# Performance work log

Measured on AMD Instinct MI355X. Metric: run time of the kernel, lower is better.

The kernel has to match this reference:

```python
import jax, jax.numpy as jnp
import numpy as np

L_MAX = 6
R = 1
IN_IRREPS  = [(256,0),(128,1),(128,2),(64,3),(64,4),(64,5),(64,6)]
HID_IRREPS = [(64,0),(64,1),(64,2),(32,3),(32,4),(32,5),(32,6)]
N_SCALARS = 64
N_GATES = sum(m for m, l in HID_IRREPS if l > 0)  # 256
PRE_IRREPS = [(N_SCALARS,0),(N_GATES,0)] + [(m,l) for m,l in HID_IRREPS if l > 0]
OUT_IRREPS = [(R,l) for l in range(L_MAX+1)]

def _dim(irr):
    return sum(m*(2*l+1) for m, l in irr)

def _wsize(in_irr, out_irr):
    mul_in = {l: m for m, l in in_irr}
    return sum(mul_in[l]*mo for mo, l in out_irr)

def e3linear(x, wflat, in_irr, out_irr):
    # block-diagonal per-irrep linear with e3nn 1/sqrt(fan_in) normalization
    B = x.shape[0]
    blocks = {}
    off = 0
    for mul, l in in_irr:
        d = mul*(2*l+1)
        blocks[l] = (x[:, off:off+d].reshape(B, mul, 2*l+1), mul)
        off += d
    outs = []
    woff = 0
    for mul_out, l in out_irr:
        xb, mul_in = blocks[l]
        w = wflat[woff:woff+mul_in*mul_out].reshape(mul_in, mul_out)
        woff += mul_in*mul_out
        y = jnp.einsum('bim,io->bom', xb, w) * (1.0/np.sqrt(mul_in))
        outs.append(y.reshape(B, mul_out*(2*l+1)))
    return jnp.concatenate(outs, axis=1)

def gate(z):
    # z = [scalars 64x0e | gates 256x0e | gated l>0 irreps]
    s = jax.nn.silu(z[:, :N_SCALARS])
    g = jax.nn.sigmoid(z[:, N_SCALARS:N_SCALARS+N_GATES])
    x = z[:, N_SCALARS+N_GATES:]
    outs = [s]
    goff = 0
    xoff = 0
    for mul, l in HID_IRREPS:
        if l == 0:
            continue
        m = 2*l+1
        xb = x[:, xoff:xoff+mul*m].reshape(-1, mul, m)
        outs.append((xb * g[:, goff:goff+mul, None]).reshape(-1, mul*m))
        goff += mul
        xoff += mul*m
    return jnp.concatenate(outs, axis=1)

def _forward(v_raw, w1, w2, w3, w4):
    x = gate(e3linear(v_raw, w1, IN_IRREPS, PRE_IRREPS))
    x = gate(e3linear(x, w2, HID_IRREPS, PRE_IRREPS))
    x = gate(e3linear(x, w3, HID_IRREPS, PRE_IRREPS))
    c = e3linear(x, w4, HID_IRREPS, OUT_IRREPS)  # [B, 49]
    B = c.shape[0]
    segs = []
    off = 0
    for l in range(L_MAX+1):
        m = 2*l+1
        seg = c[:, off:off+R*m].reshape(B, R, m).transpose(0, 2, 1)  # (B, m, R)
        segs.append(seg)
        off += R*m
    return jnp.concatenate(segs, axis=1)  # (B, 49, R)

def setup_inputs():
    key = jax.random.key(0)
    ks = jax.random.split(key, 5)
    B = 16384
    return {
        "v_raw": jax.random.normal(ks[0], (B, _dim(IN_IRREPS)), jnp.float32),
        "w1": jax.random.normal(ks[1], (_wsize(IN_IRREPS, PRE_IRREPS),), jnp.float32),
        "w2": jax.random.normal(ks[2], (_wsize(HID_IRREPS, PRE_IRREPS),), jnp.float32),
        "w3": jax.random.normal(ks[3], (_wsize(HID_IRREPS, PRE_IRREPS),), jnp.float32),
        "w4": jax.random.normal(ks[4], (_wsize(HID_IRREPS, OUT_IRREPS),), jnp.float32),
    }

def reference(v_raw, w1, w2, w3, w4):
    return _forward(v_raw, w1, w2, w3, w4)
```

## Files before the change

kernel.cpp:

```cpp
#include <hip/hip_runtime.h>
#include <cstddef>


typedef _Float16 half8 __attribute__((ext_vector_type(8)));
typedef _Float16 half4 __attribute__((ext_vector_type(4)));
typedef float    f32x4 __attribute__((ext_vector_type(4)));
typedef float    fvec4 __attribute__((ext_vector_type(4)));

#define B_ROWS   16
#define IN_DIM   3840
#define OUT_COLS 49
#define GP  264
#define HSP 72

#define OFF_G1  0
#define OFF_G2  4224
#define OFF_G3  8448
#define OFF_HS1 12672
#define OFF_HS2 13824
#define SMEM_ELTS 14976

#define P2BASE 106496
#define P3BASE 139264

__global__ __launch_bounds__(256) void prep_weights(
    const float* __restrict__ w1, const float* __restrict__ w2,
    const float* __restrict__ w3, _Float16* __restrict__ packed)
{
  static const int K_[24]    = {256,256,128,128,64,64,64,64,  64,64,64,64,32,32,32,32,
                                64,64,64,64,32,32,32,32};
  static const int N_[24]    = {64,256,64,64,32,32,32,32,  64,256,64,64,32,32,32,32,
                                64,256,64,64,32,32,32,32};
  static const int woff_[24] = {0,16384,81920,90112,98304,100352,102400,104448,
                                0,4096,20480,24576,28672,29696,30720,31744,
                                0,4096,20480,24576,28672,29696,30720,31744};
  static const int poff_[24] = {0,16384,81920,90112,98304,100352,102400,104448,
                                106496,110592,126976,131072,135168,136192,137216,138240,
                                139264,143360,159744,163840,167936,168960,169984,171008};
  const int g = blockIdx.x * 256 + threadIdx.x;
  int bi = 0;
#pragma unroll
  for (int i = 1; i < 24; ++i) if (g * 8 >= poff_[i]) bi = i;
  const float* w = (bi < 8) ? w1 : ((bi < 16) ? w2 : w3);
  const int rel8 = g - poff_[bi] / 8;
  const int K = K_[bi], N = N_[bi];
  const float scale = 1.0f / sqrtf((float)K);
  half8 vv;
  if (bi < 8) {
    const int lane = rel8 & 63;
    const int fi   = rel8 >> 6;
    const int KF = K >> 5;
    const int kf = fi % KF;
    const int mt = fi / KF;
    const int k0 = kf * 32 + (lane >> 4) * 8;
    const int o  = mt * 16 + (lane & 15);
#pragma unroll
    for (int j = 0; j < 8; ++j)
      vv[j] = (_Float16)(w[woff_[bi] + (size_t)(k0 + j) * N + o] * scale);
  } else {
    const int f  = rel8 >> 5;
    const int lp = (rel8 & 31) << 1;
    const int KF16 = K >> 4;
    const int ks = f % KF16;
    const int mt = f / KF16;
#pragma unroll
    for (int t = 0; t < 2; ++t) {
      const int l  = lp + t;
      const int i0 = ks * 16 + (l >> 4) * 4;
      const int o  = mt * 16 + (l & 15);
#pragma unroll
      for (int j = 0; j < 4; ++j)
        vv[t * 4 + j] = (_Float16)(w[woff_[bi] + (size_t)(i0 + j) * N + o] * scale);
    }
  }
  *(half8*)(packed + (size_t)g * 8) = vv;
}

template<int L> struct CP {
  static constexpr int TWOL1 = 2 * L + 1;
  static constexpr int K1  = (L <= 2) ? 128 : 64;
  static constexpr int N1  = (L <= 2) ? 64  : 32;
  static constexpr int KF1 = K1 / 32;
  static constexpr int MT  = N1 / 16;
  static constexpr int INOFF = (L==1)?256:(L==2)?640:(L==3)?1280:(L==4)?1728:(L==5)?2304:3008;
  static constexpr int P1    = (L==1)?81920:(L==2)?90112:(L==3)?98304:(L==4)?100352:(L==5)?102400:104448;
  static constexpr int P2R   = (L==1)?20480:(L==2)?24576:(L==3)?28672:(L==4)?29696:(L==5)?30720:31744;
  static constexpr int GO    = (L==1)?0:(L==2)?64:(L==3)?128:(L==4)?160:(L==5)?192:224;
  static constexpr int W4O   = (L==1)?64:(L==2)?128:(L==3)?192:(L==4)?224:(L==5)?256:288;
  static constexpr float SCALE = (N1 == 64) ? 0.125f : 0.17677669529663687f;
};

template<int L>
__device__ __forceinline__ void unit_load(const float* __restrict__ vraw,
                                          int b0, int ct, float (&tmp)[CP<L>::KF1 * 8])
{
  using P = CP<L>;
  const int lane = threadIdx.x & 63;
  const int col  = lane & 15;
  const int quad = lane >> 4;
  const int c = ct * 16 + col;
  const int b = c / P::TWOL1;
  const int m = c - b * P::TWOL1;
  const float* base = vraw + (size_t)(b0 + b) * IN_DIM + P::INOFF + m
                    + (size_t)(quad * 8) * P::TWOL1;
#pragma unroll
  for (int kf = 0; kf < P::KF1; ++kf)
#pragma unroll
    for (int j = 0; j < 8; ++j)
      tmp[kf * 8 + j] = base[(size_t)(kf * 32 + j) * P::TWOL1];
}

template<int L>
__device__ __forceinline__ void cvt_frags(const float (&tmp)[CP<L>::KF1 * 8],
                                          half8 (&bf)[CP<L>::KF1])
{
#pragma unroll
  for (int kf = 0; kf < CP<L>::KF1; ++kf)
#pragma unroll
    for (int j = 0; j < 8; ++j) bf[kf][j] = (_Float16)tmp[kf * 8 + j];
}


template<int L>
__device__ __forceinline__ void unit_compute(
    const half8 (&bf)[CP<L>::KF1], const _Float16* __restrict__ pk,
    const _Float16* G1, const _Float16* G2, const _Float16* G3,
    const float* __restrict__ w4, float* __restrict__ out, int b0, int ct)
{
  using P = CP<L>;
  const int lane = threadIdx.x & 63;
  const int col  = lane & 15;
  const int quad = lane >> 4;
  const int c = ct * 16 + col;
  const int b = c / P::TWOL1;
  const int m = c - b * P::TWOL1;

  half4 ph1[P::MT];
#pragma unroll
  for (int mt = 0; mt < P::MT; ++mt) {
    f32x4 acc = {0.f, 0.f, 0.f, 0.f};
#pragma unroll
    for (int kf = 0; kf < P::KF1; ++kf) {
      const half8 av = *(const half8*)(pk + P::P1 + (size_t)((mt * P::KF1 + kf) * 64 + lane) * 8);
      acc = __builtin_amdgcn_mfma_f32_16x16x32_f16(av, bf[kf], acc, 0, 0, 0);
    }
    const int o0 = mt * 16 + quad * 4;
    const half4 g4 = *(const half4*)(G1 + b * GP + P::GO + o0);
    half4 h;
#pragma unroll
    for (int r = 0; r < 4; ++r) h[r] = (_Float16)(acc[r] * (float)g4[r]);
    ph1[mt] = h;
  }

  half4 ph2[P::MT];
#pragma unroll
  for (int mt = 0; mt < P::MT; ++mt) {
    f32x4 acc = {0.f, 0.f, 0.f, 0.f};
#pragma unroll
    for (int ks = 0; ks < P::MT; ++ks) {
      const half4 av = *(const half4*)(pk + P2BASE + P::P2R + (size_t)((mt * P::MT + ks) * 64 + lane) * 4);
      acc = __builtin_amdgcn_mfma_f32_16x16x16f16(av, ph1[ks], acc, 0, 0, 0);
    }
    const int o0 = mt * 16 + quad * 4;
    const half4 g4 = *(const half4*)(G2 + b * GP + P::GO + o0);
    half4 h;
#pragma unroll
    for (int r = 0; r < 4; ++r) h[r] = (_Float16)(acc[r] * (float)g4[r]);
    ph2[mt] = h;
  }

  float s = 0.f;
#pragma unroll
  for (int mt = 0; mt < P::MT; ++mt) {
    f32x4 acc = {0.f, 0.f, 0.f, 0.f};
#pragma unroll
    for (int ks = 0; ks < P::MT; ++ks) {
      const half4 av = *(const half4*)(pk + P3BASE + P::P2R + (size_t)((mt * P::MT + ks) * 64 + lane) * 4);
      acc = __builtin_amdgcn_mfma_f32_16x16x16f16(av, ph2[ks], acc, 0, 0, 0);
    }
    const int o0 = mt * 16 + quad * 4;
    const half4 g4 = *(const half4*)(G3 + b * GP + P::GO + o0);
#pragma unroll
    for (int r = 0; r < 4; ++r)
      s += acc[r] * (float)g4[r] * w4[P::W4O + o0 + r];
  }
  s += __shfl_xor(s, 16, 64);
  s += __shfl_xor(s, 32, 64);
  if (quad == 0)
    out[(size_t)(b0 + b) * OUT_COLS + L * L + m] = s * P::SCALE;
}

template<int L>
__device__ __forceinline__ void unit_compute_reg(
    const half8 (&bf)[CP<L>::KF1],
    const half8 (&aw1)[CP<L>::MT * CP<L>::KF1],
    const half4 (&aw2)[CP<L>::MT * CP<L>::MT],
    const half4 (&aw3)[CP<L>::MT * CP<L>::MT],
    const _Float16* G1, const _Float16* G2, const _Float16* G3,
    const float* __restrict__ w4, float* __restrict__ out, int b0, int ct)
{
  using P = CP<L>;
  const int lane = threadIdx.x & 63;
  const int col  = lane & 15;
  const int quad = lane >> 4;
  const int c = ct * 16 + col;
  const int b = c / P::TWOL1;
  const int m = c - b * P::TWOL1;

  half4 ph1[P::MT];
#pragma unroll
  for (int mt = 0; mt < P::MT; ++mt) {
    f32x4 acc = {0.f, 0.f, 0.f, 0.f};
#pragma unroll
    for (int kf = 0; kf < P::KF1; ++kf)
      acc = __builtin_amdgcn_mfma_f32_16x16x32_f16(aw1[mt * P::KF1 + kf], bf[kf], acc, 0, 0, 0);
    const int o0 = mt * 16 + quad * 4;
    const half4 g4 = *(const half4*)(G1 + b * GP + P::GO + o0);
    half4 h;
#pragma unroll
    for (int r = 0; r < 4; ++r) h[r] = (_Float16)(acc[r] * (float)g4[r]);
    ph1[mt] = h;
  }

  half4 ph2[P::MT];
#pragma unroll
  for (int mt = 0; mt < P::MT; ++mt) {
    f32x4 acc = {0.f, 0.f, 0.f, 0.f};
#pragma unroll
    for (int ks = 0; ks < P::MT; ++ks)
      acc = __builtin_amdgcn_mfma_f32_16x16x16f16(aw2[mt * P::MT + ks], ph1[ks], acc, 0, 0, 0);
    const int o0 = mt * 16 + quad * 4;
    const half4 g4 = *(const half4*)(G2 + b * GP + P::GO + o0);
    half4 h;
#pragma unroll
    for (int r = 0; r < 4; ++r) h[r] = (_Float16)(acc[r] * (float)g4[r]);
    ph2[mt] = h;
  }

  float s = 0.f;
#pragma unroll
  for (int mt = 0; mt < P::MT; ++mt) {
    f32x4 acc = {0.f, 0.f, 0.f, 0.f};
#pragma unroll
    for (int ks = 0; ks < P::MT; ++ks)
      acc = __builtin_amdgcn_mfma_f32_16x16x16f16(aw3[mt * P::MT + ks], ph2[ks], acc, 0, 0, 0);
    const int o0 = mt * 16 + quad * 4;
    const half4 g4 = *(const half4*)(G3 + b * GP + P::GO + o0);
#pragma unroll
    for (int r = 0; r < 4; ++r)
      s += acc[r] * (float)g4[r] * w4[P::W4O + o0 + r];
  }
  s += __shfl_xor(s, 16, 64);
  s += __shfl_xor(s, 32, 64);
  if (quad == 0)
    out[(size_t)(b0 + b) * OUT_COLS + L * L + m] = s * P::SCALE;
}

template<int L, int CT0, int NCT>
__device__ __forceinline__ void run_chain(
    const float* __restrict__ vraw, const _Float16* __restrict__ pk,
    const _Float16* G1, const _Float16* G2, const _Float16* G3,
    const float* __restrict__ w4, float* __restrict__ out, int b0)
{
  using P = CP<L>;
  float tmp[P::KF1 * 8];
  unit_load<L>(vraw, b0, CT0, tmp);
  if constexpr (L >= 3) {
    const int lane = threadIdx.x & 63;
    half8 aw1[P::MT * P::KF1];
    half4 aw2[P::MT * P::MT];
    half4 aw3[P::MT * P::MT];
#pragma unroll
    for (int f = 0; f < P::MT * P::KF1; ++f)
      aw1[f] = *(const half8*)(pk + P::P1 + (size_t)(f * 64 + lane) * 8);
#pragma unroll
    for (int f = 0; f < P::MT * P::MT; ++f) {
      aw2[f] = *(const half4*)(pk + P2BASE + P::P2R + (size_t)(f * 64 + lane) * 4);
      aw3[f] = *(const half4*)(pk + P3BASE + P::P2R + (size_t)(f * 64 + lane) * 4);
    }
#pragma unroll 1
    for (int u = 0; u < NCT; ++u) {
      half8 bf[P::KF1];
      cvt_frags<L>(tmp, bf);
      if (u + 1 < NCT) unit_load<L>(vraw, b0, CT0 + u + 1, tmp);
      unit_compute_reg<L>(bf, aw1, aw2, aw3, G1, G2, G3, w4, out, b0, CT0 + u);
    }
  } else {
#pragma unroll 1
    for (int u = 0; u < NCT; ++u) {
      half8 bf[P::KF1];
      cvt_frags<L>(tmp, bf);
      if (u + 1 < NCT) unit_load<L>(vraw, b0, CT0 + u + 1, tmp);
      unit_compute<L>(bf, pk, G1, G2, G3, w4, out, b0, CT0 + u);
    }
  }
}

__device__ __forceinline__ void load_scal_frags(const float* __restrict__ vraw,
                                                int b0, half8 (&sf)[8])
{
  const int lane = threadIdx.x & 63;
  const int col  = lane & 15;
  const int quad = lane >> 4;
  const float* base = vraw + (size_t)(b0 + col) * IN_DIM + quad * 8;
#pragma unroll
  for (int kf = 0; kf < 8; ++kf) {
    const fvec4 a = *(const fvec4*)(base + kf * 32);
    const fvec4 b2 = *(const fvec4*)(base + kf * 32 + 4);
#pragma unroll
    for (int j = 0; j < 4; ++j) { sf[kf][j] = (_Float16)a[j]; sf[kf][4 + j] = (_Float16)b2[j]; }
  }
}

__device__ __forceinline__ void scal_L1(const half8 (&sf)[8],
    const _Float16* __restrict__ pk, _Float16* Hs1, _Float16* G1v)
{
  const int lane = threadIdx.x & 63;
  const int wv   = threadIdx.x >> 6;
  const int col  = lane & 15;
  const int quad = lane >> 4;
  {
    f32x4 acc = {0.f, 0.f, 0.f, 0.f};
#pragma unroll
    for (int kf = 0; kf < 8; ++kf) {
      const half8 av = *(const half8*)(pk + (size_t)((wv * 8 + kf) * 64 + lane) * 8);
      acc = __builtin_amdgcn_mfma_f32_16x16x32_f16(av, sf[kf], acc, 0, 0, 0);
    }
    const int o0 = wv * 16 + quad * 4;
    half4 h;
#pragma unroll
    for (int r = 0; r < 4; ++r) { const float z = acc[r]; h[r] = (_Float16)(z / (1.f + __expf(-z))); }
    *(half4*)(Hs1 + col * HSP + o0) = h;
  }
#pragma unroll
  for (int t = 0; t < 4; ++t) {
    const int mt = wv * 4 + t;
    f32x4 acc = {0.f, 0.f, 0.f, 0.f};
#pragma unroll
    for (int kf = 0; kf < 8; ++kf) {
      const half8 av = *(const half8*)(pk + 16384 + (size_t)((mt * 8 + kf) * 64 + lane) * 8);
      acc = __builtin_amdgcn_mfma_f32_16x16x32_f16(av, sf[kf], acc, 0, 0, 0);
    }
    const int o0 = mt * 16 + quad * 4;
    half4 g;
#pragma unroll
    for (int r = 0; r < 4; ++r) g[r] = (_Float16)(1.f / (1.f + __expf(-acc[r])));
    *(half4*)(G1v + col * GP + o0) = g;
  }
}

__device__ __forceinline__ void scal_mid(const _Float16* HsIn,
    const _Float16* __restrict__ pkS, const _Float16* __restrict__ pkG,
    _Float16* HsOut, _Float16* Gv)
{
  const int lane = threadIdx.x & 63;
  const int wv   = threadIdx.x >> 6;
  const int col  = lane & 15;
  const int quad = lane >> 4;
  half4 bf4[4];
#pragma unroll
  for (int ks = 0; ks < 4; ++ks)
    bf4[ks] = *(const half4*)(HsIn + col * HSP + ks * 16 + quad * 4);
  {
    f32x4 acc = {0.f, 0.f, 0.f, 0.f};
#pragma unroll
    for (int ks = 0; ks < 4; ++ks) {
      const half4 av = *(const half4*)(pkS + (size_t)((wv * 4 + ks) * 64 + lane) * 4);
      acc = __builtin_amdgcn_mfma_f32_16x16x16f16(av, bf4[ks], acc, 0, 0, 0);
    }
    const int o0 = wv * 16 + quad * 4;
    half4 h;
#pragma unroll
    for (int r = 0; r < 4; ++r) { const float z = acc[r]; h[r] = (_Float16)(z / (1.f + __expf(-z))); }
    *(half4*)(HsOut + col * HSP + o0) = h;
  }
#pragma unroll
  for (int t = 0; t < 4; ++t) {
    const int mt = wv * 4 + t;
    f32x4 acc = {0.f, 0.f, 0.f, 0.f};
#pragma unroll
    for (int ks = 0; ks < 4; ++ks) {
      const half4 av = *(const half4*)(pkG + (size_t)((mt * 4 + ks) * 64 + lane) * 4);
      acc = __builtin_amdgcn_mfma_f32_16x16x16f16(av, bf4[ks], acc, 0, 0, 0);
    }
    const int o0 = mt * 16 + quad * 4;
    half4 g;
#pragma unroll
    for (int r = 0; r < 4; ++r) g[r] = (_Float16)(1.f / (1.f + __expf(-acc[r])));
    *(half4*)(Gv + col * GP + o0) = g;
  }
}

__device__ __forceinline__ void scal_last(const _Float16* Hs2,
    const _Float16* __restrict__ pkS, const _Float16* __restrict__ pkG,
    _Float16* G3v, const float* __restrict__ w4, float* __restrict__ out, int b0)
{
  const int lane = threadIdx.x & 63;
  const int wv   = threadIdx.x >> 6;
  const int col  = lane & 15;
  const int quad = lane >> 4;
  half4 bf4[4];
#pragma unroll
  for (int ks = 0; ks < 4; ++ks)
    bf4[ks] = *(const half4*)(Hs2 + col * HSP + ks * 16 + quad * 4);
  if (wv == 0) {
    float s = 0.f;
#pragma unroll
    for (int mt = 0; mt < 4; ++mt) {
      f32x4 acc = {0.f, 0.f, 0.f, 0.f};
#pragma unroll
      for (int ks = 0; ks < 4; ++ks) {
        const half4 av = *(const half4*)(pkS + (size_t)((mt * 4 + ks) * 64 + lane) * 4);
        acc = __builtin_amdgcn_mfma_f32_16x16x16f16(av, bf4[ks], acc, 0, 0, 0);
      }
      const int o0 = mt * 16 + quad * 4;
#pragma unroll
      for (int r = 0; r < 4; ++r) {
        const float z = acc[r];
        s += (z / (1.f + __expf(-z))) * w4[o0 + r];
      }
    }
    s += __shfl_xor(s, 16, 64);
    s += __shfl_xor(s, 32, 64);
    if (quad == 0) out[(size_t)(b0 + col) * OUT_COLS] = s * 0.125f;
  } else {
    const int t0 = (wv == 1) ? 0 : (wv == 2) ? 6 : 11;
    const int tn = (wv == 1) ? 6 : 5;
    for (int t = 0; t < tn; ++t) {
      const int mt = t0 + t;
      f32x4 acc = {0.f, 0.f, 0.f, 0.f};
#pragma unroll
      for (int ks = 0; ks < 4; ++ks) {
        const half4 av = *(const half4*)(pkG + (size_t)((mt * 4 + ks) * 64 + lane) * 4);
        acc = __builtin_amdgcn_mfma_f32_16x16x16f16(av, bf4[ks], acc, 0, 0, 0);
      }
      const int o0 = mt * 16 + quad * 4;
      half4 g;
#pragma unroll
      for (int r = 0; r < 4; ++r) g[r] = (_Float16)(1.f / (1.f + __expf(-acc[r])));
      *(half4*)(G3v + col * GP + o0) = g;
    }
  }
}

__global__ __launch_bounds__(256, 3) void fused_decoder(
    const float* __restrict__ vraw, const float* __restrict__ w4,
    const _Float16* __restrict__ pk, float* __restrict__ out)
{
  __shared__ __align__(16) _Float16 smem[SMEM_ELTS];
  _Float16* G1  = smem + OFF_G1;
  _Float16* G2  = smem + OFF_G2;
  _Float16* G3  = smem + OFF_G3;
  _Float16* Hs1 = smem + OFF_HS1;
  _Float16* Hs2 = smem + OFF_HS2;
  const int wv = threadIdx.x >> 6;
  const int b0 = blockIdx.x * B_ROWS;

  half8 sf[8];
  load_scal_frags(vraw, b0, sf);
  scal_L1(sf, pk, Hs1, G1);
  __syncthreads();
  scal_mid(Hs1, pk + P2BASE, pk + P2BASE + 4096, Hs2, G2);
  __syncthreads();
  scal_last(Hs2, pk + P3BASE, pk + P3BASE + 4096, G3, w4, out, b0);
  __syncthreads();

  if (wv == 0) {
    run_chain<2, 0, 5>(vraw, pk, G1, G2, G3, w4, out, b0);
    run_chain<3, 0, 4>(vraw, pk, G1, G2, G3, w4, out, b0);
  } else if (wv == 1) {
    run_chain<1, 0, 3>(vraw, pk, G1, G2, G3, w4, out, b0);
    run_chain<3, 4, 3>(vraw, pk, G1, G2, G3, w4, out, b0);
    run_chain<4, 0, 5>(vraw, pk, G1, G2, G3, w4, out, b0);
  } else if (wv == 2) {
    run_chain<6, 0, 13>(vraw, pk, G1, G2, G3, w4, out, b0);
    run_chain<4, 5, 1>(vraw, pk, G1, G2, G3, w4, out, b0);
  } else {
    run_chain<5, 0, 11>(vraw, pk, G1, G2, G3, w4, out, b0);
    run_chain<4, 6, 3>(vraw, pk, G1, G2, G3, w4, out, b0);
  }
}

extern "C" void kernel_launch(void* const* d_in, const int* in_sizes, int n_in,
                              void* d_out, int out_size, void* d_ws, size_t ws_size,
                              hipStream_t stream)
{
  (void)in_sizes; (void)n_in; (void)out_size; (void)ws_size;
  const float* vraw = (const float*)d_in[0];
  const float* w1   = (const float*)d_in[1];
  const float* w2   = (const float*)d_in[2];
  const float* w3   = (const float*)d_in[3];
  const float* w4   = (const float*)d_in[4];
  float* out = (float*)d_out;
  _Float16* packed = (_Float16*)d_ws;

  prep_weights<<<84, 256, 0, stream>>>(w1, w2, w3, packed);
  fused_decoder<<<16384 / B_ROWS, 256, 0, stream>>>(vraw, w4, packed, out);
}
```

Baseline: 408.6 us.

## Stage L>=3 input tiles through per-wave LDS with coalesced float4 loads

For the L>=3 chains, each wave now loads the input rows it needs as contiguous float4 chunks into a per-wave LDS scratch area, then gathers the strided MFMA B-fragments from LDS instead of doing scalar strided global loads. The next tile's global load is issued before compute and written to LDS after it, keeping the prefetch overlap. This raises LDS use to about 70 KB per block, so launch bounds drop from 3 to 2 blocks per CU, trading occupancy for more coalesced global traffic.

```diff
diff --git a/kernel.cpp b/kernel.cpp
--- a/kernel.cpp
+++ b/kernel.cpp
@@ -18,7 +18,9 @@
 #define OFF_G3  8448
 #define OFF_HS1 12672
 #define OFF_HS2 13824
-#define SMEM_ELTS 14976
+#define OFF_SCR 14976
+#define SCRW_F  2560
+#define SMEM_ELTS 35456
 
 #define P2BASE 106496
 #define P3BASE 139264
@@ -120,6 +122,71 @@
     for (int j = 0; j < 8; ++j) bf[kf][j] = (_Float16)tmp[kf * 8 + j];
 }
 
+template<int L> struct SG {
+  static constexpr int NW   = CP<L>::TWOL1 * 64;
+  static constexpr int NW4  = CP<L>::TWOL1 * 16;
+  static constexpr int MAXROWS = (L == 3) ? 4 : 3;
+  static constexpr int MAXIT = (NW4 * MAXROWS + 63) / 64;
+};
+
+template<int L>
+__device__ __forceinline__ void stage_issue(const float* __restrict__ vraw,
+    int b0, int ct, fvec4 (&rv)[SG<L>::MAXIT])
+{
+  using P = CP<L>;
+  const int lane = threadIdx.x & 63;
+  const int blo = (ct * 16) / P::TWOL1;
+  const int bhi = (ct * 16 + 15) / P::TWOL1;
+  const int chunks = SG<L>::NW4 * (bhi - blo + 1);
+  const float* base = vraw + (size_t)(b0 + blo) * IN_DIM + P::INOFF;
+#pragma unroll
+  for (int it = 0; it < SG<L>::MAXIT; ++it) {
+    int t = it * 64 + lane;
+    t = (t < chunks) ? t : (chunks - 1);
+    const int r = t / SG<L>::NW4;
+    const int o = t - r * SG<L>::NW4;
+    rv[it] = *(const fvec4*)(base + (size_t)r * IN_DIM + o * 4);
+  }
+}
+
+template<int L>
+__device__ __forceinline__ void stage_write(const fvec4 (&rv)[SG<L>::MAXIT],
+    float* scr, int ct)
+{
+  using P = CP<L>;
+  const int lane = threadIdx.x & 63;
+  const int blo = (ct * 16) / P::TWOL1;
+  const int bhi = (ct * 16 + 15) / P::TWOL1;
+  const int chunks = SG<L>::NW4 * (bhi - blo + 1);
+#pragma unroll
+  for (int it = 0; it < SG<L>::MAXIT; ++it) {
+    int t = it * 64 + lane;
+    t = (t < chunks) ? t : (chunks - 1);
+    const int r = t / SG<L>::NW4;
+    const int o = t - r * SG<L>::NW4;
+    *(fvec4*)(scr + r * SG<L>::NW + o * 4) = rv[it];
+  }
+}
+
+template<int L>
+__device__ __forceinline__ void read_frags(const float* scr, int ct,
+                                           half8 (&bf)[CP<L>::KF1])
+{
+  using P = CP<L>;
+  const int lane = threadIdx.x & 63;
+  const int col  = lane & 15;
+  const int quad = lane >> 4;
+  const int c = ct * 16 + col;
+  const int blo = (ct * 16) / P::TWOL1;
+  const int b = c / P::TWOL1;
+  const int m = c - b * P::TWOL1;
+  const float* base = scr + (b - blo) * SG<L>::NW + m + quad * 8 * P::TWOL1;
+#pragma unroll
+  for (int kf = 0; kf < P::KF1; ++kf)
+#pragma unroll
+    for (int j = 0; j < 8; ++j)
+      bf[kf][j] = (_Float16)base[(kf * 32 + j) * P::TWOL1];
+}
 
 template<int L>
 __device__ __forceinline__ void unit_compute(
@@ -265,34 +332,45 @@
   using P = CP<L>;
   float tmp[P::KF1 * 8];
   unit_load<L>(vraw, b0, CT0, tmp);
-  if constexpr (L >= 3) {
-    const int lane = threadIdx.x & 63;
-    half8 aw1[P::MT * P::KF1];
-    half4 aw2[P::MT * P::MT];
-    half4 aw3[P::MT * P::MT];
-#pragma unroll
-    for (int f = 0; f < P::MT * P::KF1; ++f)
-      aw1[f] = *(const half8*)(pk + P::P1 + (size_t)(f * 64 + lane) * 8);
-#pragma unroll
-    for (int f = 0; f < P::MT * P::MT; ++f) {
-      aw2[f] = *(const half4*)(pk + P2BASE + P::P2R + (size_t)(f * 64 + lane) * 4);
-      aw3[f] = *(const half4*)(pk + P3BASE + P::P2R + (size_t)(f * 64 + lane) * 4);
-    }
 #pragma unroll 1
-    for (int u = 0; u < NCT; ++u) {
-      half8 bf[P::KF1];
-      cvt_frags<L>(tmp, bf);
-      if (u + 1 < NCT) unit_load<L>(vraw, b0, CT0 + u + 1, tmp);
-      unit_compute_reg<L>(bf, aw1, aw2, aw3, G1, G2, G3, w4, out, b0, CT0 + u);
-    }
-  } else {
+  for (int u = 0; u < NCT; ++u) {
+    half8 bf[P::KF1];
+    cvt_frags<L>(tmp, bf);
+    if (u + 1 < NCT) unit_load<L>(vraw, b0, CT0 + u + 1, tmp);
+    unit_compute<L>(bf, pk, G1, G2, G3, w4, out, b0, CT0 + u);
+  }
+}
+
+template<int L, int CT0, int NCT>
+__device__ __forceinline__ void run_chain_staged(
+    const float* __restrict__ vraw, const _Float16* __restrict__ pk,
+    const _Float16* G1, const _Float16* G2, const _Float16* G3,
+    const float* __restrict__ w4, float* __restrict__ out, int b0, float* scr)
+{
+  using P = CP<L>;
+  const int lane = threadIdx.x & 63;
+  half8 aw1[P::MT * P::KF1];
+  half4 aw2[P::MT * P::MT];
+  half4 aw3[P::MT * P::MT];
+#pragma unroll
+  for (int f = 0; f < P::MT * P::KF1; ++f)
+    aw1[f] = *(const half8*)(pk + P::P1 + (size_t)(f * 64 + lane) * 8);
+#pragma unroll
+  for (int f = 0; f < P::MT * P::MT; ++f) {
+    aw2[f] = *(const half4*)(pk + P2BASE + P::P2R + (size_t)(f * 64 + lane) * 4);
+    aw3[f] = *(const half4*)(pk + P3BASE + P::P2R + (size_t)(f * 64 + lane) * 4);
+  }
+
+  fvec4 rv[SG<L>::MAXIT];
+  stage_issue<L>(vraw, b0, CT0, rv);
+  stage_write<L>(rv, scr, CT0);
 #pragma unroll 1
-    for (int u = 0; u < NCT; ++u) {
-      half8 bf[P::KF1];
-      cvt_frags<L>(tmp, bf);
-      if (u + 1 < NCT) unit_load<L>(vraw, b0, CT0 + u + 1, tmp);
-      unit_compute<L>(bf, pk, G1, G2, G3, w4, out, b0, CT0 + u);
-    }
+  for (int u = 0; u < NCT; ++u) {
+    half8 bf[P::KF1];
+    read_frags<L>(scr, CT0 + u, bf);
+    if (u + 1 < NCT) stage_issue<L>(vraw, b0, CT0 + u + 1, rv);
+    unit_compute_reg<L>(bf, aw1, aw2, aw3, G1, G2, G3, w4, out, b0, CT0 + u);
+    if (u + 1 < NCT) stage_write<L>(rv, scr, CT0 + u + 1);
   }
 }
 
@@ -443,7 +521,7 @@
   }
 }
 
-__global__ __launch_bounds__(256, 3) void fused_decoder(
+__global__ __launch_bounds__(256, 2) void fused_decoder(
     const float* __restrict__ vraw, const float* __restrict__ w4,
     const _Float16* __restrict__ pk, float* __restrict__ out)
 {
@@ -454,6 +532,7 @@
   _Float16* Hs1 = smem + OFF_HS1;
   _Float16* Hs2 = smem + OFF_HS2;
   const int wv = threadIdx.x >> 6;
+  float* scrw = (float*)(smem + OFF_SCR) + wv * SCRW_F;
   const int b0 = blockIdx.x * B_ROWS;
 
   half8 sf[8];
@@ -467,17 +546,17 @@
 
   if (wv == 0) {
     run_chain<2, 0, 5>(vraw, pk, G1, G2, G3, w4, out, b0);
-    run_chain<3, 0, 4>(vraw, pk, G1, G2, G3, w4, out, b0);
+    run_chain_staged<3, 0, 4>(vraw, pk, G1, G2, G3, w4, out, b0, scrw);
   } else if (wv == 1) {
     run_chain<1, 0, 3>(vraw, pk, G1, G2, G3, w4, out, b0);
-    run_chain<3, 4, 3>(vraw, pk, G1, G2, G3, w4, out, b0);
-    run_chain<4, 0, 5>(vraw, pk, G1, G2, G3, w4, out, b0);
+    run_chain_staged<3, 4, 3>(vraw, pk, G1, G2, G3, w4, out, b0, scrw);
+    run_chain_staged<4, 0, 5>(vraw, pk, G1, G2, G3, w4, out, b0, scrw);
   } else if (wv == 2) {
-    run_chain<6, 0, 13>(vraw, pk, G1, G2, G3, w4, out, b0);
-    run_chain<4, 5, 1>(vraw, pk, G1, G2, G3, w4, out, b0);
+    run_chain_staged<6, 0, 13>(vraw, pk, G1, G2, G3, w4, out, b0, scrw);
+    run_chain_staged<4, 5, 1>(vraw, pk, G1, G2, G3, w4, out, b0, scrw);
   } else {
-    run_chain<5, 0, 11>(vraw, pk, G1, G2, G3, w4, out, b0);
-    run_chain<4, 6, 3>(vraw, pk, G1, G2, G3, w4, out, b0);
+    run_chain_staged<5, 0, 11>(vraw, pk, G1, G2, G3, w4, out, b0, scrw);
+    run_chain_staged<4, 6, 3>(vraw, pk, G1, G2, G3, w4, out, b0, scrw);
   }
 }
 
```

Result: faster. 377.9 us (-7.5%).
